# Performance work log

Hardware: AMD Instinct MI355X
Metric: run time of the kernel (lower is better)

Reference implementation:

```python
import jax, jax.numpy as jnp
import numpy as np

B = 2048   # batch size
D = 2048   # feature dim (ResNet-50)
H = 2048   # projection hidden dim
T = 0.1    # temperature
EPS_BN = 1e-5
CC_ITERS = 32  # >= ~2*log2(B), enough for pointer-jumping convergence


def setup_inputs() -> dict:
    key = jax.random.key(0)
    ks = jax.random.split(key, 4)
    s = 0.02
    return {
        "x1": jax.random.normal(ks[0], (B, D), dtype=jnp.float32),
        "x2": jax.random.normal(ks[1], (B, D), dtype=jnp.float32),
        "W1": jax.random.normal(ks[2], (H, D), dtype=jnp.float32) * s,
        "b1": jnp.zeros((H,), jnp.float32),
        "gamma": jnp.ones((H,), jnp.float32),
        "beta": jnp.zeros((H,), jnp.float32),
        "W2": jax.random.normal(ks[3], (D, H), dtype=jnp.float32) * s,
        "b2": jnp.zeros((D,), jnp.float32),
    }


def _head(x, W1, b1, gamma, beta, W2, b2):
    # ProjectionHead: Linear -> BatchNorm1d (train mode, batch stats) -> ReLU -> Linear
    h = x @ W1.T + b1
    mu = h.mean(0)
    var = h.var(0)  # biased variance, as torch BN uses for normalization
    h = (h - mu) * jax.lax.rsqrt(var + EPS_BN) * gamma + beta
    h = jax.nn.relu(h)
    o = h @ W2.T + b2
    n = jnp.maximum(jnp.linalg.norm(o, axis=1, keepdims=True), 1e-12)
    return o / n  # F.normalize


def _cc_mask(feat):
    # build_connected_component: kNN(k=1) graph + connected components -> same-label mask
    b = feat.shape[0]
    sim = jax.lax.stop_gradient(feat @ feat.T) - 2.0 * jnp.eye(b, dtype=feat.dtype)
    y = jnp.argmax(sim, axis=1)  # topk(1) neighbor per row
    # min-label propagation with pointer jumping (GPU-native union-find equivalent)
    def body(_, l):
        ln = jnp.minimum(l, l[y])      # propagate along edge i -> y[i]
        ln = ln.at[y].min(l)           # propagate along reverse edge y[i] -> i
        return jnp.minimum(ln, ln[ln])  # pointer jumping
    labels = jax.lax.fori_loop(0, CC_ITERS, body, jnp.arange(b))
    return (labels[:, None] == labels[None, :]).astype(feat.dtype)


def _sup_contra(logits, mask, diag):
    dm = 1.0 - diag
    mask = mask * dm
    exp_logits = jnp.exp(logits) * dm
    log_prob = logits - jnp.log(exp_logits.sum(1, keepdims=True))
    mean_log_prob_pos = (mask * log_prob).sum(1) / mask.sum(1)
    return (-mean_log_prob_pos).mean()


def reference(x1, x2, W1, b1, gamma, beta, W2, b2):
    # Only head2 branch contributes to the returned graph_loss (head1 branch is dead code
    # w.r.t. the return value), so we compute exactly the graph_loss path.
    feat1 = _head(x1, W1, b1, gamma, beta, W2, b2)
    feat2 = _head(x2, W1, b1, gamma, beta, W2, b2)
    mask1 = _cc_mask(feat1)
    mask2 = _cc_mask(feat2)
    diag = jnp.eye(B, dtype=feat1.dtype)
    loss = _sup_contra(feat1 @ feat1.T / T, mask2, diag)
    loss = loss + _sup_contra(feat2 @ feat2.T / T, mask1, diag)
    return loss / 2.0
```

## Files before the change

### kernel.cpp

```cpp
#include <hip/hip_runtime.h>
#include <hip/hip_bf16.h>

typedef __bf16 bf16_t;
typedef __bf16 bf16x4 __attribute__((ext_vector_type(4)));
typedef __bf16 bf16x8 __attribute__((ext_vector_type(8)));
typedef float  f32x4  __attribute__((ext_vector_type(4)));

__device__ __forceinline__ void gload_lds16(const void* g, void* l)
{
    __builtin_amdgcn_global_load_lds((__attribute__((address_space(1))) void*)g,
                                     (__attribute__((address_space(3))) void*)l,
                                     16, 0, 0);
}

__global__ __launch_bounds__(256) void cast_all(const float* __restrict__ x1, const float* __restrict__ x2,
                                                const float* __restrict__ W1, const float* __restrict__ W2,
                                                bf16_t* __restrict__ xcatb, bf16_t* __restrict__ W1b,
                                                bf16_t* __restrict__ W2b)
{
    const size_t i  = ((size_t)blockIdx.x * 256 + threadIdx.x) * 4;
    const size_t M4 = 1ull << 22;
    const size_t r  = i >> 22;
    const size_t off = i & (M4 - 1);
    const float* src; bf16_t* dst;
    if (r == 0)      { src = x1; dst = xcatb; }
    else if (r == 1) { src = x2; dst = xcatb + M4; }
    else if (r == 2) { src = W1; dst = W1b; }
    else             { src = W2; dst = W2b; }
    f32x4 v = *(const f32x4*)(src + off);
    bf16x4 o;
    o[0] = (bf16_t)v[0]; o[1] = (bf16_t)v[1]; o[2] = (bf16_t)v[2]; o[3] = (bf16_t)v[3];
    *(bf16x4*)(dst + off) = o;
}

__global__ __launch_bounds__(512, 1) void gemm8b(
    const bf16_t* __restrict__ A, const bf16_t* __restrict__ B,
    const float* __restrict__ bias, bf16_t* __restrict__ C,
    long long b_batch_stride, int mode,
    float* __restrict__ ps, float* __restrict__ ps2,
    float* __restrict__ rsq, const float* __restrict__ rnv,
    unsigned long long* __restrict__ pkey, float* __restrict__ lseP)
{
    __shared__ bf16_t lsA[4][256 * 32];
    __shared__ bf16_t lsB[4][128 * 32];
    __shared__ float  cs2[8][64], cq2[8][64];
    __shared__ float  rq2[8][64];
    __shared__ float  ls2[8][64];
    __shared__ unsigned long long kv2[8][64];
    const int tid  = threadIdx.x;
    const int lane = tid & 63;
    const int wave = tid >> 6;
    const int l15  = lane & 15;
    const int cg   = lane >> 4;
    const int wm   = (wave >> 1) * 64;
    const int wn   = (wave & 1) * 64;
    const int m0   = blockIdx.y * 256;
    const int n0   = blockIdx.x * 128;
    const int K = 2048, N = 2048, NT = 32;
    const bf16_t* Bb = B + (size_t)(m0 >> 11) * b_batch_stride;

    f32x4 acc[4][4] = {};

    auto STAGE_A = [&](int k0, bf16_t* dst) {
#pragma unroll
        for (int i = 0; i < 2; ++i) {
            const int ch  = wave * 128 + i * 64 + lane;
            const int row = ch >> 2;
            const int cs  = ((ch & 3) - ((row >> 1) & 3)) & 3;
            gload_lds16(A + (size_t)(m0 + row) * K + k0 + cs * 8, dst + ch * 8);
        }
    };
    auto STAGE_B = [&](int k0, bf16_t* dst) {
        const int ch  = wave * 64 + lane;
        const int row = ch >> 2;
        const int cs  = ((ch & 3) - ((row >> 1) & 3)) & 3;
        gload_lds16(Bb + (size_t)(n0 + row) * K + k0 + cs * 8, dst + ch * 8);
    };
    auto FRAG = [&](const bf16_t* u, int row) -> bf16x8 {
        const int p = (cg + (row >> 1)) & 3;
        return *(const bf16x8*)&u[row * 32 + p * 8];
    };

    STAGE_A(0,  lsA[0]); STAGE_B(0,  lsB[0]);
    STAGE_A(32, lsA[1]); STAGE_B(32, lsB[1]);
    asm volatile("s_waitcnt vmcnt(3)" ::: "memory");
    __builtin_amdgcn_sched_barrier(0);
    __builtin_amdgcn_s_barrier();

    for (int t = 0; t < NT; ++t) {
        const int s0 = (2 * t) & 3, s1 = (2 * t + 1) & 3;
        const int s2 = (2 * t + 2) & 3, s3 = (2 * t + 3) & 3;
        const bool st = (t < NT - 1);
        const int kn = (t + 1) * 64;
        bf16x8 af[4], bfr[4];

#pragma unroll
        for (int f = 0; f < 4; ++f) af[f]  = FRAG(lsA[s0], wm + f * 16 + l15);
#pragma unroll
        for (int f = 0; f < 4; ++f) bfr[f] = FRAG(lsB[s0], wn + f * 16 + l15);
        if (st) { STAGE_A(kn, lsA[s2]); STAGE_B(kn, lsB[s2]);
                  asm volatile("s_waitcnt vmcnt(3)" ::: "memory"); }
        else      asm volatile("s_waitcnt vmcnt(0)" ::: "memory");
        __builtin_amdgcn_sched_barrier(0);
        __builtin_amdgcn_s_barrier();
        __builtin_amdgcn_sched_barrier(0);
        __builtin_amdgcn_s_setprio(1);
#pragma unroll
        for (int fm = 0; fm < 4; ++fm)
#pragma unroll
            for (int fn = 0; fn < 4; ++fn)
                acc[fm][fn] = __builtin_amdgcn_mfma_f32_16x16x32_bf16(af[fm], bfr[fn], acc[fm][fn], 0, 0, 0);
        __builtin_amdgcn_s_setprio(0);

#pragma unroll
        for (int f = 0; f < 4; ++f) af[f]  = FRAG(lsA[s1], wm + f * 16 + l15);
#pragma unroll
        for (int f = 0; f < 4; ++f) bfr[f] = FRAG(lsB[s1], wn + f * 16 + l15);
        if (st) { STAGE_A(kn + 32, lsA[s3]); STAGE_B(kn + 32, lsB[s3]);
                  asm volatile("s_waitcnt vmcnt(3)" ::: "memory"); }
        __builtin_amdgcn_sched_barrier(0);
        __builtin_amdgcn_s_barrier();
        __builtin_amdgcn_sched_barrier(0);
        __builtin_amdgcn_s_setprio(1);
#pragma unroll
        for (int fm = 0; fm < 4; ++fm)
#pragma unroll
            for (int fn = 0; fn < 4; ++fn)
                acc[fm][fn] = __builtin_amdgcn_mfma_f32_16x16x32_bf16(af[fm], bfr[fn], acc[fm][fn], 0, 0, 0);
        __builtin_amdgcn_s_setprio(0);
    }
    __syncthreads();

    if (mode == 2) {
        const int rnb = (m0 >> 11) * 2048;
#pragma unroll
        for (int fm = 0; fm < 4; ++fm) {
            const int mb = m0 + wm + fm * 16 + cg * 4;
            const f32x4 rm = *(const f32x4*)&rnv[mb];
#pragma unroll
            for (int fn = 0; fn < 4; ++fn) {
                const float rc = rnv[rnb + n0 + wn + fn * 16 + l15];
#pragma unroll
                for (int r = 0; r < 4; ++r)
                    acc[fm][fn][r] *= rm[r] * rc;
            }
        }
    }

#pragma unroll
    for (int fm = 0; fm < 4; ++fm) {
        const int rb = m0 + wm + fm * 16 + cg * 4;
#pragma unroll
        for (int fn = 0; fn < 4; ++fn) {
            const int colg = n0 + wn + fn * 16 + l15;
            const float bv = bias ? bias[colg] : 0.0f;
#pragma unroll
            for (int r = 0; r < 4; ++r)
                C[(size_t)(rb + r) * N + colg] = (bf16_t)(acc[fm][fn][r] + bv);
        }
    }

    if (mode == 1) {
#pragma unroll
        for (int fn = 0; fn < 4; ++fn) {
            const int cl = fn * 16 + l15;
            const float bv = bias[n0 + wn + cl];
            float s = 0.f, q = 0.f;
#pragma unroll
            for (int fm = 0; fm < 4; ++fm)
#pragma unroll
                for (int r = 0; r < 4; ++r) {
                    const float v = acc[fm][fn][r] + bv;
                    s += v; q += v * v;
                }
            s += __shfl_xor(s, 16); q += __shfl_xor(q, 16);
            s += __shfl_xor(s, 32); q += __shfl_xor(q, 32);
            if (lane < 16) { cs2[wave][cl] = s; cq2[wave][cl] = q; }
        }
        __syncthreads();
        if (tid < 128) {
            const int p = tid >> 6, cl = tid & 63;
            ps [(size_t)blockIdx.y * 2048 + n0 + tid] =
                cs2[p][cl] + cs2[p + 2][cl] + cs2[p + 4][cl] + cs2[p + 6][cl];
            ps2[(size_t)blockIdx.y * 2048 + n0 + tid] =
                cq2[p][cl] + cq2[p + 2][cl] + cq2[p + 4][cl] + cq2[p + 6][cl];
        }
    } else if (mode == 3) {
#pragma unroll
        for (int fm = 0; fm < 4; ++fm)
#pragma unroll
            for (int r = 0; r < 4; ++r) {
                float q = 0.f;
#pragma unroll
                for (int fn = 0; fn < 4; ++fn) {
                    const float v = acc[fm][fn][r] + bias[n0 + wn + fn * 16 + l15];
                    q += v * v;
                }
                q += __shfl_xor(q, 1); q += __shfl_xor(q, 2);
                q += __shfl_xor(q, 4); q += __shfl_xor(q, 8);
                if (l15 == 0) rq2[wave][fm * 16 + cg * 4 + r] = q;
            }
        __syncthreads();
        if (tid < 256) {
            const int mg = tid >> 6, rl = tid & 63;
            rsq[(size_t)blockIdx.x * 4096 + m0 + tid] = rq2[2 * mg][rl] + rq2[2 * mg + 1][rl];
        }
    } else if (mode == 2) {
#pragma unroll
        for (int fm = 0; fm < 4; ++fm)
#pragma unroll
            for (int r = 0; r < 4; ++r) {
                const int rl   = fm * 16 + cg * 4 + r;
                const int self = (m0 + wm + rl) & 2047;
                float best = -1.0e38f; int bi = 0x7fffffff; float se = 0.f;
#pragma unroll
                for (int fn = 0; fn < 4; ++fn) {
                    const int cgl = n0 + wn + fn * 16 + l15;
                    const float v = acc[fm][fn][r];
                    if (cgl != self) {
                        se += expf(10.0f * v);
                        if (v > best) { best = v; bi = cgl; }
                    }
                }
#pragma unroll
                for (int st2 = 1; st2 <= 8; st2 <<= 1) {
                    const float ov = __shfl_xor(best, st2);
                    const int   oi = __shfl_xor(bi, st2);
                    if (ov > best || (ov == best && oi < bi)) { best = ov; bi = oi; }
                    se += __shfl_xor(se, st2);
                }
                if (l15 == 0) {
                    unsigned u = __float_as_uint(best);
                    u = (u & 0x80000000u) ? ~u : (u | 0x80000000u);
                    kv2[wave][rl] = ((unsigned long long)u << 32) | (unsigned)(~bi);
                    ls2[wave][rl] = se;
                }
            }
        __syncthreads();
        if (tid < 256) {
            const int mg = tid >> 6, rl = tid & 63;
            const unsigned long long a = kv2[2 * mg][rl], b = kv2[2 * mg + 1][rl];
            pkey[(size_t)blockIdx.x * 4096 + m0 + tid] = a > b ? a : b;
            lseP[(size_t)blockIdx.x * 4096 + m0 + tid] = ls2[2 * mg][rl] + ls2[2 * mg + 1][rl];
        }
    }
}

__global__ __launch_bounds__(256) void bn_final2(const float* __restrict__ ps, const float* __restrict__ ps2,
                                                 float* __restrict__ mu, float* __restrict__ rinv)
{
    const int c = blockIdx.x * 256 + threadIdx.x;
    const int b = c >> 11, col = c & 2047;
    float s = 0.f, s2 = 0.f;
    for (int i = 0; i < 8; ++i) {
        s  += ps [(size_t)(b * 8 + i) * 2048 + col];
        s2 += ps2[(size_t)(b * 8 + i) * 2048 + col];
    }
    const float m = s * (1.0f / 2048.0f);
    const float v = s2 * (1.0f / 2048.0f) - m * m;
    mu[c]   = m;
    rinv[c] = rsqrtf(v + 1e-5f);
}

__global__ __launch_bounds__(256) void bn_apply(const bf16_t* __restrict__ h, const float* __restrict__ mu,
                                                const float* __restrict__ rinv, const float* __restrict__ gamma,
                                                const float* __restrict__ beta, bf16_t* __restrict__ out)
{
    const size_t base = ((size_t)blockIdx.x * 256 + threadIdx.x) * 8;
    const int col = (int)(base & 2047);
    const int br  = (int)(base >> 22);
    bf16x8 v = *(const bf16x8*)(h + base);
    bf16x8 o;
#pragma unroll
    for (int j = 0; j < 8; ++j) {
        const int c = col + j;
        const float f = (float)v[j];
        const float t = (f - mu[br * 2048 + c]) * rinv[br * 2048 + c] * gamma[c] + beta[c];
        o[j] = (bf16_t)fmaxf(t, 0.0f);
    }
    *(bf16x8*)(out + base) = o;
}

__global__ __launch_bounds__(256) void norm_final(const float* __restrict__ rsq, float* __restrict__ rn)
{
    const int r = blockIdx.x * 256 + threadIdx.x;
    float s = 0.f;
    for (int nb = 0; nb < 16; ++nb) s += rsq[(size_t)nb * 4096 + r];
    rn[r] = 1.0f / fmaxf(sqrtf(s), 1e-12f);
}

__global__ __launch_bounds__(1024) void cc_labels(const unsigned long long* __restrict__ pkey,
                                                  int* __restrict__ labg)
{
    __shared__ int A_[2048];
    __shared__ int Bn[2048];
    __shared__ int Y_[2048];
    __shared__ int chg;
    const int br = blockIdx.x;
    const int t = threadIdx.x;
    if (t == 0) chg = 0;
    for (int i = t; i < 2048; i += 1024) {
        const int row = br * 2048 + i;
        unsigned long long k = 0ull;
        for (int nb = 0; nb < 16; ++nb) {
            const unsigned long long v = pkey[(size_t)nb * 4096 + row];
            k = (v > k) ? v : k;
        }
        Y_[i] = (int)~((unsigned)(k & 0xFFFFFFFFull));
        A_[i] = i;
    }
    __syncthreads();
    for (int it = 0; it < 32; ++it) {
        for (int i = t; i < 2048; i += 1024) Bn[i] = min(A_[i], A_[Y_[i]]);
        __syncthreads();
        for (int i = t; i < 2048; i += 1024) atomicMin(&Bn[Y_[i]], A_[i]);
        __syncthreads();
        int ch = 0;
        for (int i = t; i < 2048; i += 1024) {
            const int b = Bn[i];
            const int nv = min(b, Bn[b]);
            if (nv != A_[i]) { ch = 1; A_[i] = nv; }
        }
        if (ch) atomicOr(&chg, 1);
        __syncthreads();
        const int c = chg;
        __syncthreads();
        if (t == 0) chg = 0;
        if (!c) break;
    }
    for (int i = t; i < 2048; i += 1024) labg[br * 2048 + i] = A_[i];
}

__global__ __launch_bounds__(256) void loss_rows(const bf16_t* __restrict__ simb, const int* __restrict__ labels,
                                                 const float* __restrict__ lseP, float* __restrict__ terms)
{
    const int row = blockIdx.x;
    const int br  = row >> 11;
    const int* lab = labels + ((1 - br) << 11);
    const int self = row & 2047;
    const int li = lab[self];
    const int t = threadIdx.x;
    const bf16x8 v8 = *(const bf16x8*)(simb + (size_t)row * 2048 + t * 8);
    float psum = 0.f; int pc = 0;
#pragma unroll
    for (int j = 0; j < 8; ++j) {
        const int c = t * 8 + j;
        if (c == self) continue;
        if (lab[c] == li) { psum += 10.0f * (float)v8[j]; pc++; }
    }
    __shared__ float PS[256]; __shared__ int PC[256];
    PS[t] = psum; PC[t] = pc;
    __syncthreads();
    for (int off = 128; off; off >>= 1) {
        if (t < off) { PS[t] += PS[t + off]; PC[t] += PC[t + off]; }
        __syncthreads();
    }
    if (t == 0) {
        float se = 0.f;
        for (int nb = 0; nb < 16; ++nb) se += lseP[(size_t)nb * 4096 + row];
        terms[row] = logf(se) - PS[0] / (float)PC[0];
    }
}

__global__ __launch_bounds__(1024) void final_reduce(const float* __restrict__ terms, float* __restrict__ out)
{
    const int t = threadIdx.x;
    float s = terms[t] + terms[t + 1024] + terms[t + 2048] + terms[t + 3072];
    __shared__ float S[1024];
    S[t] = s;
    __syncthreads();
    for (int off = 512; off; off >>= 1) { if (t < off) S[t] += S[t + off]; __syncthreads(); }
    if (t == 0) out[0] = S[0] * (1.0f / 4096.0f);
}

extern "C" void kernel_launch(void* const* d_in, const int* in_sizes, int n_in,
                              void* d_out, int out_size, void* d_ws, size_t ws_size,
                              hipStream_t stream)
{
    const float* x1    = (const float*)d_in[0];
    const float* x2    = (const float*)d_in[1];
    const float* W1    = (const float*)d_in[2];
    const float* b1    = (const float*)d_in[3];
    const float* gamma = (const float*)d_in[4];
    const float* beta  = (const float*)d_in[5];
    const float* W2    = (const float*)d_in[6];
    const float* b2    = (const float*)d_in[7];

    char* ws = (char*)d_ws;
    const size_t MB = 1024ull * 1024ull;
    const size_t NN = 2048ull * 2048ull;
    bf16_t* W1b    = (bf16_t*)(ws + 0);
    bf16_t* W2b    = (bf16_t*)(ws + 8 * MB);
    bf16_t* xcatb  = (bf16_t*)(ws + 16 * MB);
    bf16_t* hnb    = (bf16_t*)(ws + 16 * MB);
    bf16_t* hb16   = (bf16_t*)(ws + 32 * MB);
    bf16_t* ob16   = (bf16_t*)(ws + 64 * MB);
    bf16_t* simb   = (bf16_t*)(ws + 0);
    float*  psA    = (float*)(ws + 80 * MB);
    float*  psB    = psA + 32 * 2048;
    float*  rsq    = psB + 32 * 2048;
    float*  mu     = rsq + 16 * 4096;
    float*  rinv   = mu + 4096;
    float*  rn     = rinv + 4096;
    float*  lseP   = rn + 4096;
    unsigned long long* pkey = (unsigned long long*)(lseP + 16 * 4096);
    int*    labels = (int*)(pkey + 16 * 4096);
    float*  terms  = (float*)(labels + 4096);

    cast_all<<<16384, 256, 0, stream>>>(x1, x2, W1, W2, xcatb, W1b, W2b);

    gemm8b<<<dim3(16, 16), 512, 0, stream>>>(xcatb, W1b, b1, hb16, 0, 1,
                                             psA, psB, nullptr, nullptr, nullptr, nullptr);
    bn_final2<<<16, 256, 0, stream>>>(psA, psB, mu, rinv);
    bn_apply<<<4096, 256, 0, stream>>>(hb16, mu, rinv, gamma, beta, hnb);

    gemm8b<<<dim3(16, 16), 512, 0, stream>>>(hnb, W2b, b2, ob16, 0, 3,
                                             nullptr, nullptr, rsq, nullptr, nullptr, nullptr);
    norm_final<<<16, 256, 0, stream>>>(rsq, rn);

    gemm8b<<<dim3(16, 16), 512, 0, stream>>>(ob16, ob16, nullptr, simb, (long long)NN, 2,
                                             nullptr, nullptr, nullptr, rn, pkey, lseP);

    cc_labels<<<2, 1024, 0, stream>>>(pkey, labels);
    loss_rows<<<4096, 256, 0, stream>>>(simb, labels, lseP, terms);
    final_reduce<<<1, 1024, 0, stream>>>(terms, (float*)d_out);
}
```

Before: 205.3 us.

## Switch GEMM to three-stage LDS ring with aliased epilogue scratch

```diff
diff --git a/kernel.cpp b/kernel.cpp
--- a/kernel.cpp
+++ b/kernel.cpp
@@ -33,7 +33,7 @@
     *(bf16x4*)(dst + off) = o;
 }
 
-__global__ __launch_bounds__(512, 1) void gemm8b(
+__global__ __launch_bounds__(512, 4) void gemm8d(
     const bf16_t* __restrict__ A, const bf16_t* __restrict__ B,
     const float* __restrict__ bias, bf16_t* __restrict__ C,
     long long b_batch_stride, int mode,
@@ -41,12 +41,8 @@
     float* __restrict__ rsq, const float* __restrict__ rnv,
     unsigned long long* __restrict__ pkey, float* __restrict__ lseP)
 {
-    __shared__ bf16_t lsA[4][256 * 32];
-    __shared__ bf16_t lsB[4][128 * 32];
-    __shared__ float  cs2[8][64], cq2[8][64];
-    __shared__ float  rq2[8][64];
-    __shared__ float  ls2[8][64];
-    __shared__ unsigned long long kv2[8][64];
+    __shared__ __align__(16) char smem[73728];
+    bf16_t* ring = (bf16_t*)smem;
     const int tid  = threadIdx.x;
     const int lane = tid & 63;
     const int wave = tid >> 6;
@@ -56,7 +52,7 @@
     const int wn   = (wave & 1) * 64;
     const int m0   = blockIdx.y * 256;
     const int n0   = blockIdx.x * 128;
-    const int K = 2048, N = 2048, NT = 32;
+    const int K = 2048, N = 2048;
     const bf16_t* Bb = B + (size_t)(m0 >> 11) * b_batch_stride;
 
     f32x4 acc[4][4] = {};
@@ -81,29 +77,27 @@
         return *(const bf16x8*)&u[row * 32 + p * 8];
     };
 
-    STAGE_A(0,  lsA[0]); STAGE_B(0,  lsB[0]);
-    STAGE_A(32, lsA[1]); STAGE_B(32, lsB[1]);
-    asm volatile("s_waitcnt vmcnt(3)" ::: "memory");
-    __builtin_amdgcn_sched_barrier(0);
-    __builtin_amdgcn_s_barrier();
-
-    for (int t = 0; t < NT; ++t) {
-        const int s0 = (2 * t) & 3, s1 = (2 * t + 1) & 3;
-        const int s2 = (2 * t + 2) & 3, s3 = (2 * t + 3) & 3;
-        const bool st = (t < NT - 1);
-        const int kn = (t + 1) * 64;
-        bf16x8 af[4], bfr[4];
-
-#pragma unroll
-        for (int f = 0; f < 4; ++f) af[f]  = FRAG(lsA[s0], wm + f * 16 + l15);
-#pragma unroll
-        for (int f = 0; f < 4; ++f) bfr[f] = FRAG(lsB[s0], wn + f * 16 + l15);
-        if (st) { STAGE_A(kn, lsA[s2]); STAGE_B(kn, lsB[s2]);
-                  asm volatile("s_waitcnt vmcnt(3)" ::: "memory"); }
-        else      asm volatile("s_waitcnt vmcnt(0)" ::: "memory");
+    STAGE_A(0, ring);
+    STAGE_B(0, ring + 8192);
+
+    for (int p = 0; p < 64; ++p) {
+        bf16_t* uA = ring + (p % 3) * 12288;
+        bf16_t* uB = uA + 8192;
+        if (p < 63) {
+            bf16_t* nA = ring + ((p + 1) % 3) * 12288;
+            STAGE_A((p + 1) * 32, nA);
+            STAGE_B((p + 1) * 32, nA + 8192);
+            asm volatile("s_waitcnt vmcnt(3)" ::: "memory");
+        } else {
+            asm volatile("s_waitcnt vmcnt(0)" ::: "memory");
+        }
         __builtin_amdgcn_sched_barrier(0);
         __builtin_amdgcn_s_barrier();
-        __builtin_amdgcn_sched_barrier(0);
+        bf16x8 af[4], bfr[4];
+#pragma unroll
+        for (int f = 0; f < 4; ++f) af[f]  = FRAG(uA, wm + f * 16 + l15);
+#pragma unroll
+        for (int f = 0; f < 4; ++f) bfr[f] = FRAG(uB, wn + f * 16 + l15);
         __builtin_amdgcn_s_setprio(1);
 #pragma unroll
         for (int fm = 0; fm < 4; ++fm)
@@ -111,23 +105,6 @@
             for (int fn = 0; fn < 4; ++fn)
                 acc[fm][fn] = __builtin_amdgcn_mfma_f32_16x16x32_bf16(af[fm], bfr[fn], acc[fm][fn], 0, 0, 0);
         __builtin_amdgcn_s_setprio(0);
-
-#pragma unroll
-        for (int f = 0; f < 4; ++f) af[f]  = FRAG(lsA[s1], wm + f * 16 + l15);
-#pragma unroll
-        for (int f = 0; f < 4; ++f) bfr[f] = FRAG(lsB[s1], wn + f * 16 + l15);
-        if (st) { STAGE_A(kn + 32, lsA[s3]); STAGE_B(kn + 32, lsB[s3]);
-                  asm volatile("s_waitcnt vmcnt(3)" ::: "memory"); }
-        __builtin_amdgcn_sched_barrier(0);
-        __builtin_amdgcn_s_barrier();
-        __builtin_amdgcn_sched_barrier(0);
-        __builtin_amdgcn_s_setprio(1);
-#pragma unroll
-        for (int fm = 0; fm < 4; ++fm)
-#pragma unroll
-            for (int fn = 0; fn < 4; ++fn)
-                acc[fm][fn] = __builtin_amdgcn_mfma_f32_16x16x32_bf16(af[fm], bfr[fn], acc[fm][fn], 0, 0, 0);
-        __builtin_amdgcn_s_setprio(0);
     }
     __syncthreads();
 
@@ -161,6 +138,8 @@
     }
 
     if (mode == 1) {
+        float* cs2 = (float*)smem;
+        float* cq2 = cs2 + 512;
 #pragma unroll
         for (int fn = 0; fn < 4; ++fn) {
             const int cl = fn * 16 + l15;
@@ -175,17 +154,18 @@
                 }
             s += __shfl_xor(s, 16); q += __shfl_xor(q, 16);
             s += __shfl_xor(s, 32); q += __shfl_xor(q, 32);
-            if (lane < 16) { cs2[wave][cl] = s; cq2[wave][cl] = q; }
+            if (lane < 16) { cs2[wave * 64 + cl] = s; cq2[wave * 64 + cl] = q; }
         }
         __syncthreads();
         if (tid < 128) {
             const int p = tid >> 6, cl = tid & 63;
             ps [(size_t)blockIdx.y * 2048 + n0 + tid] =
-                cs2[p][cl] + cs2[p + 2][cl] + cs2[p + 4][cl] + cs2[p + 6][cl];
+                cs2[p * 64 + cl] + cs2[(p + 2) * 64 + cl] + cs2[(p + 4) * 64 + cl] + cs2[(p + 6) * 64 + cl];
             ps2[(size_t)blockIdx.y * 2048 + n0 + tid] =
-                cq2[p][cl] + cq2[p + 2][cl] + cq2[p + 4][cl] + cq2[p + 6][cl];
+                cq2[p * 64 + cl] + cq2[(p + 2) * 64 + cl] + cq2[(p + 4) * 64 + cl] + cq2[(p + 6) * 64 + cl];
         }
     } else if (mode == 3) {
+        float* rq2 = (float*)smem;
 #pragma unroll
         for (int fm = 0; fm < 4; ++fm)
 #pragma unroll
@@ -198,14 +178,17 @@
                 }
                 q += __shfl_xor(q, 1); q += __shfl_xor(q, 2);
                 q += __shfl_xor(q, 4); q += __shfl_xor(q, 8);
-                if (l15 == 0) rq2[wave][fm * 16 + cg * 4 + r] = q;
+                if (l15 == 0) rq2[wave * 64 + fm * 16 + cg * 4 + r] = q;
             }
         __syncthreads();
         if (tid < 256) {
             const int mg = tid >> 6, rl = tid & 63;
-            rsq[(size_t)blockIdx.x * 4096 + m0 + tid] = rq2[2 * mg][rl] + rq2[2 * mg + 1][rl];
+            rsq[(size_t)blockIdx.x * 4096 + m0 + tid] =
+                rq2[2 * mg * 64 + rl] + rq2[(2 * mg + 1) * 64 + rl];
         }
     } else if (mode == 2) {
+        float* ls2 = (float*)smem;
+        unsigned long long* kv2 = (unsigned long long*)(smem + 4096);
 #pragma unroll
         for (int fm = 0; fm < 4; ++fm)
 #pragma unroll
@@ -232,16 +215,17 @@
                 if (l15 == 0) {
                     unsigned u = __float_as_uint(best);
                     u = (u & 0x80000000u) ? ~u : (u | 0x80000000u);
-                    kv2[wave][rl] = ((unsigned long long)u << 32) | (unsigned)(~bi);
-                    ls2[wave][rl] = se;
+                    kv2[wave * 64 + rl] = ((unsigned long long)u << 32) | (unsigned)(~bi);
+                    ls2[wave * 64 + rl] = se;
                 }
             }
         __syncthreads();
         if (tid < 256) {
             const int mg = tid >> 6, rl = tid & 63;
-            const unsigned long long a = kv2[2 * mg][rl], b = kv2[2 * mg + 1][rl];
+            const unsigned long long a = kv2[2 * mg * 64 + rl], b = kv2[(2 * mg + 1) * 64 + rl];
             pkey[(size_t)blockIdx.x * 4096 + m0 + tid] = a > b ? a : b;
-            lseP[(size_t)blockIdx.x * 4096 + m0 + tid] = ls2[2 * mg][rl] + ls2[2 * mg + 1][rl];
+            lseP[(size_t)blockIdx.x * 4096 + m0 + tid] =
+                ls2[2 * mg * 64 + rl] + ls2[(2 * mg + 1) * 64 + rl];
         }
     }
 }
@@ -409,16 +393,16 @@
 
     cast_all<<<16384, 256, 0, stream>>>(x1, x2, W1, W2, xcatb, W1b, W2b);
 
-    gemm8b<<<dim3(16, 16), 512, 0, stream>>>(xcatb, W1b, b1, hb16, 0, 1,
+    gemm8d<<<dim3(16, 16), 512, 0, stream>>>(xcatb, W1b, b1, hb16, 0, 1,
                                              psA, psB, nullptr, nullptr, nullptr, nullptr);
     bn_final2<<<16, 256, 0, stream>>>(psA, psB, mu, rinv);
     bn_apply<<<4096, 256, 0, stream>>>(hb16, mu, rinv, gamma, beta, hnb);
 
-    gemm8b<<<dim3(16, 16), 512, 0, stream>>>(hnb, W2b, b2, ob16, 0, 3,
+    gemm8d<<<dim3(16, 16), 512, 0, stream>>>(hnb, W2b, b2, ob16, 0, 3,
                                              nullptr, nullptr, rsq, nullptr, nullptr, nullptr);
     norm_final<<<16, 256, 0, stream>>>(rsq, rn);
 
-    gemm8b<<<dim3(16, 16), 512, 0, stream>>>(ob16, ob16, nullptr, simb, (long long)NN, 2,
+    gemm8d<<<dim3(16, 16), 512, 0, stream>>>(ob16, ob16, nullptr, simb, (long long)NN, 2,
                                              nullptr, nullptr, nullptr, rn, pkey, lseP);
 
     cc_labels<<<2, 1024, 0, stream>>>(pkey, labels);
```

After: 203.7 us (median of 2 runs). Within noise of the previous version (-0.8%).
